# Kernel tuning notes

Measured on AMD Instinct MI355X. Metric: run time of the kernel, lower is better.

The kernel has to match this reference:

```python
import jax, jax.numpy as jnp
import numpy as np

COMMITMENT_COST = 0.25
NUM_EMBEDDINGS = 512
EMBEDDING_DIM = 128


def setup_inputs() -> dict:
    key = jax.random.key(0)
    k1, k2 = jax.random.split(key)
    z = jax.random.normal(k1, (64, 128, 32, 32), dtype=jnp.float32)
    # nn.Embedding weight initialized uniform(-1/K, 1/K)
    lim = 1.0 / NUM_EMBEDDINGS
    emb_weight = jax.random.uniform(
        k2, (NUM_EMBEDDINGS, EMBEDDING_DIM), dtype=jnp.float32,
        minval=-lim, maxval=lim)
    return {"z": z, "emb_weight": emb_weight}


def reference(z, emb_weight):
    b, c, h, w = z.shape  # c == embedding_dim
    # (b, h, w, c) -> (b*h*w, c)
    z_cl = jnp.transpose(z, (0, 2, 3, 1))
    z_flat = z_cl.reshape(b * h * w, c)
    # squared L2 distances: ||z||^2 + ||e||^2 - 2 z.e  -> [N, K]
    distances = (
        jnp.sum(z_flat ** 2, axis=-1, keepdims=True)
        + jnp.sum(emb_weight ** 2, axis=-1)[None, :]
        - 2.0 * jnp.matmul(z_flat, emb_weight.T)
    )
    encoding_indices = jnp.argmin(distances, axis=-1)  # [N]
    z_q = emb_weight[encoding_indices]                 # [N, c]
    z_q = z_q.reshape(b, h, w, c)
    z_q = jnp.transpose(z_q, (0, 3, 1, 2))             # [b, c, h, w]
    loss = (
        jnp.mean((z_q - jax.lax.stop_gradient(z)) ** 2)
        + COMMITMENT_COST * jnp.mean((jax.lax.stop_gradient(z_q) - z) ** 2)
    )
    # straight-through estimator
    z_q_st = z + jax.lax.stop_gradient(z_q - z)
    return (z_q_st, loss, encoding_indices)
```

## Files before the change

### kernel.cpp

```cpp
#include <hip/hip_runtime.h>


#define D_DIM 128
#define HW    1024
#define GAP_THR 4e-4f
#define FLAG_CAP 16384

typedef short short8 __attribute__((ext_vector_type(8)));
typedef float f32x16 __attribute__((ext_vector_type(16)));

union U8 { unsigned int u[4]; short8 s; uint4 q; };

__device__ __forceinline__ unsigned short f2bf(float v) {
    unsigned int u = __builtin_bit_cast(unsigned int, v);
    return (unsigned short)((u + 0x7fffu + ((u >> 16) & 1u)) >> 16);
}
__device__ __forceinline__ unsigned int umn(unsigned int a, unsigned int b) {
    return a < b ? a : b;
}
__device__ __forceinline__ unsigned int umx(unsigned int a, unsigned int b) {
    return a > b ? a : b;
}

__global__ void prep_kernel(const float* __restrict__ emb,
                            float* __restrict__ etr,
                            uint4* __restrict__ ebh,
                            float* __restrict__ se) {
    const int t = blockIdx.x * 256 + threadIdx.x;

    {
        const int k = t >> 7;
        const int d = t & 127;
        etr[d * 512 + k] = emb[t];
    }

    if (t < 8192) {
        const int lane = t & 63;
        const int ks   = (t >> 6) & 7;
        const int kcol = t >> 9;
        const int krow = kcol * 32 + (lane & 31);
        const int d0   = ks * 16 + (lane >> 5) * 8;
        const float* ep = emb + (size_t)krow * D_DIM + d0;
        float v[8];
        #pragma unroll
        for (int j = 0; j < 8; ++j) v[j] = ep[j];
        U8 hh;
        #pragma unroll
        for (int p = 0; p < 4; ++p) {
            const unsigned short h0 = f2bf(v[2*p]), h1 = f2bf(v[2*p+1]);
            hh.u[p] = (unsigned int)h0 | ((unsigned int)h1 << 16);
        }
        ebh[t] = hh.q;
    }

    if (t < 512) {
        const float* e = emb + (size_t)t * D_DIM;
        float r[8];
        #pragma unroll
        for (int j = 0; j < 8; ++j) {
            float v = e[j];
            float p = v * v;
            asm("" : "+v"(p));
            r[j] = p;
        }
        for (int i = 8; i < 128; i += 8) {
            #pragma unroll
            for (int j = 0; j < 8; ++j) {
                float v = e[i + j];
                float p = v * v;
                asm("" : "+v"(p));
                r[j] += p;
            }
        }
        se[t] = ((r[0] + r[1]) + (r[2] + r[3])) + ((r[4] + r[5]) + (r[6] + r[7]));
    }
}

__launch_bounds__(256, 4)
__global__ void dist_kernel(const float* __restrict__ z,
                            const uint4* __restrict__ ebh,
                            const float* __restrict__ se_g,
                            const float* __restrict__ emb,
                            float* __restrict__ idx_out,
                            unsigned int* __restrict__ flag_cnt,
                            int* __restrict__ flag_list,
                            float* __restrict__ zq,
                            double* __restrict__ loss) {
    __shared__ unsigned int red1[2][64], red2[2][64];
    __shared__ int   li_sh[64];
    __shared__ float ept[D_DIM * 33];
    __shared__ float lred[4];

    const int tid  = threadIdx.x;
    const int lane = tid & 63;
    const int wid  = tid >> 6;
    const int wn   = wid >> 1;
    const int wk   = wid & 1;
    const int row  = lane & 31;
    const int bidl = (int)blockIdx.x;
    const int bid  = (bidl & 7) * 128 + (bidl >> 3);
    const int nblk = bid * 64;
    const int bimg = nblk >> 10;
    const int hw0  = nblk & 1023;
    const int hww  = hw0 + wn * 32;

    short8 Ah[8];
    {
        const float* zc = z + (size_t)bimg * (D_DIM * HW) + hww + row;
        #pragma unroll
        for (int ks = 0; ks < 8; ++ks) {
            const int d0 = ks * 16 + (lane >> 5) * 8;
            float v[8];
            #pragma unroll
            for (int j = 0; j < 8; ++j) v[j] = zc[(size_t)(d0 + j) * HW];
            U8 hh;
            #pragma unroll
            for (int p = 0; p < 4; ++p) {
                unsigned int hwd;
                asm("v_cvt_pk_bf16_f32 %0, %1, %2" : "=v"(hwd) : "v"(v[2*p]), "v"(v[2*p+1]));
                hh.u[p] = hwd;
            }
            Ah[ks] = hh.s;
        }
    }

    unsigned int b1[16], b2[16];
    #pragma unroll
    for (int j = 0; j < 16; ++j) { b1[j] = 0xFFFFFFFFu; b2[j] = 0xFFFFFFFFu; }

    #pragma unroll
    for (int i = 0; i < 8; ++i) {
        const int   kc   = wk * 8 + ((i + bidl) & 7);
        const int   kgl  = kc * 32 + row;
        const float sevp = se_g[kgl] + 0.5f;
        const uint4* pbh = ebh + kc * 512 + lane;

        f32x16 acc;
        #pragma unroll
        for (int j = 0; j < 16; ++j) acc[j] = 0.f;

        __builtin_amdgcn_s_setprio(1);
        #pragma unroll
        for (int ks = 0; ks < 8; ++ks) {
            U8 bh; bh.q = pbh[ks * 64];
            acc = __builtin_amdgcn_mfma_f32_32x32x16_bf16(Ah[ks], bh.s, acc, 0, 0, 0);
        }
        __builtin_amdgcn_s_setprio(0);

        #pragma unroll
        for (int j = 0; j < 16; ++j) {
            const float pd = fmaf(-2.f, acc[j], sevp);
            const unsigned int key =
                (__builtin_bit_cast(unsigned int, pd) & 0xFFFFFE00u) | (unsigned int)kgl;
            const unsigned int m = umn(key, b1[j]);
            b2[j] = umn(umx(key, b1[j]), b2[j]);
            b1[j] = m;
        }
    }

    #pragma unroll
    for (int off = 1; off <= 16; off <<= 1) {
        #pragma unroll
        for (int j = 0; j < 16; ++j) {
            const unsigned int o1 = (unsigned int)__shfl_xor((int)b1[j], off);
            const unsigned int o2 = (unsigned int)__shfl_xor((int)b2[j], off);
            const unsigned int m  = umn(b1[j], o1);
            b2[j] = umn(umx(b1[j], o1), umn(b2[j], o2));
            b1[j] = m;
        }
    }

    if ((lane & 31) == 0) {
        const int half = lane >> 5;
        #pragma unroll
        for (int j = 0; j < 16; ++j) {
            const int r = wn * 32 + (j & 3) + 8 * (j >> 2) + 4 * half;
            red1[wk][r] = b1[j];
            red2[wk][r] = b2[j];
        }
    }
    __syncthreads();

    if (tid < 64) {
        const unsigned int v1a = red1[0][tid], v2a = red2[0][tid];
        const unsigned int v1b = red1[1][tid], v2b = red2[1][tid];
        const unsigned int m1 = umn(v1a, v1b);
        const unsigned int m2 = umn(umn(v2a, v2b), umx(v1a, v1b));
        const int n = nblk + tid;
        const int code = (int)(m1 & 511u);
        idx_out[n] = (float)code;
        li_sh[tid] = code;
        const float f1 = __builtin_bit_cast(float, m1 & 0xFFFFFE00u);
        const float f2 = __builtin_bit_cast(float, m2 & 0xFFFFFE00u);
        if (f2 - f1 < GAP_THR) {
            unsigned int p = atomicAdd(flag_cnt, 1u);
            if (p < FLAG_CAP) flag_list[p] = n;
        }
    }

    float lacc = 0.f;
    for (int h = 0; h < 2; ++h) {
        __syncthreads();
        {
            const int p   = tid >> 3;
            const int sub = tid & 7;
            const float* er = emb + (size_t)li_sh[h * 32 + p] * D_DIM + sub * 16;
            #pragma unroll
            for (int j4 = 0; j4 < 4; ++j4) {
                const float4 v = *(const float4*)(er + j4 * 4);
                const int c = sub * 16 + j4 * 4;
                ept[(c + 0) * 33 + p] = v.x;
                ept[(c + 1) * 33 + p] = v.y;
                ept[(c + 2) * 33 + p] = v.z;
                ept[(c + 3) * 33 + p] = v.w;
            }
        }
        __syncthreads();
        {
            const int p  = tid & 31;
            const int c0 = tid >> 5;
            const int hwp = hw0 + h * 32 + p;
            const float* zb2 = z  + (size_t)bimg * (D_DIM * HW) + hwp;
            float*       qb  = zq + (size_t)bimg * (D_DIM * HW) + hwp;
            #pragma unroll
            for (int i = 0; i < 16; ++i) {
                const int c = c0 + i * 8;
                const float v  = ept[c * 33 + p];
                const float zv = zb2[(size_t)c * HW];
                qb[(size_t)c * HW] = v;
                const float df = v - zv;
                lacc = fmaf(df, df, lacc);
            }
        }
    }
    #pragma unroll
    for (int off = 32; off > 0; off >>= 1) lacc += __shfl_down(lacc, off);
    if (lane == 0) lred[wid] = lacc;
    __syncthreads();
    if (tid == 0)
        atomicAdd(loss, (double)(lred[0] + lred[1] + lred[2] + lred[3]));
}

__launch_bounds__(512)
__global__ void fixup_kernel(const float* __restrict__ z,
                             const float* __restrict__ etr,
                             const unsigned int* __restrict__ flag_cnt,
                             const int* __restrict__ flag_list,
                             const float* __restrict__ se_np,
                             float* __restrict__ idx_out) {
    __shared__ float zrow[D_DIM];
    __shared__ float q[D_DIM];
    __shared__ float rsum[8];
    __shared__ float szs;
    __shared__ float rv[8];
    __shared__ int   rix[8];

    const int tid = threadIdx.x;
    unsigned int cnt = *flag_cnt;
    if (cnt > FLAG_CAP) cnt = FLAG_CAP;

    for (unsigned int f = blockIdx.x; f < cnt; f += gridDim.x) {
        const int row = flag_list[f];
        const int b   = row >> 10;
        const int hw  = row & 1023;
        __syncthreads();
        if (tid < D_DIM) {
            float v = z[(size_t)b * (D_DIM * HW) + (size_t)tid * HW + hw];
            zrow[tid] = v;
            q[tid] = v * v;
        }
        __syncthreads();
        if (tid < 8) {
            float r = q[tid];
            for (int i = 8; i < 128; i += 8) r += q[i + tid];
            rsum[tid] = r;
        }
        __syncthreads();
        if (tid == 0)
            szs = ((rsum[0] + rsum[1]) + (rsum[2] + rsum[3]))
                + ((rsum[4] + rsum[5]) + (rsum[6] + rsum[7]));
        __syncthreads();
        const float sz32 = szs;

        const int k = tid;
        double dot0 = 0.0, dot1 = 0.0;
        #pragma unroll 4
        for (int d = 0; d < D_DIM; d += 2) {
            dot0 += (double)etr[d * 512 + k]       * (double)zrow[d];
            dot1 += (double)etr[(d + 1) * 512 + k] * (double)zrow[d + 1];
        }
        const float dotf = (float)(dot0 + dot1);
        const float T    = sz32 + se_np[k];
        float best  = T - 2.0f * dotf;
        int   besti = k;

        #pragma unroll
        for (int off = 32; off > 0; off >>= 1) {
            const float ov = __shfl_down(best, off);
            const int   oi = __shfl_down(besti, off);
            if (ov < best || (ov == best && oi < besti)) { best = ov; besti = oi; }
        }
        if ((tid & 63) == 0) { rv[tid >> 6] = best; rix[tid >> 6] = besti; }
        __syncthreads();
        if (tid == 0) {
            #pragma unroll
            for (int w = 1; w < 8; ++w)
                if (rv[w] < best || (rv[w] == best && rix[w] < besti)) {
                    best = rv[w]; besti = rix[w];
                }
            idx_out[row] = (float)besti;
        }
    }
}

__global__ void fin_kernel(const double* __restrict__ loss, float* __restrict__ out_loss) {
    *out_loss = (float)(*loss * 1.25 / 8388608.0);
}

extern "C" void kernel_launch(void* const* d_in, const int* in_sizes, int n_in,
                              void* d_out, int out_size, void* d_ws, size_t ws_size,
                              hipStream_t stream) {
    const float* z   = (const float*)d_in[0];
    const float* emb = (const float*)d_in[1];
    float* out      = (float*)d_out;
    float* zq       = out;
    float* out_loss = out + 8388608;
    float* idx_f    = out + 8388609;

    char* ws = (char*)d_ws;
    unsigned int* flag_cnt = (unsigned int*)ws;
    double*       loss     = (double*)(ws + 8);
    float*        se       = (float*)(ws + 10240);
    uint4*        ebh      = (uint4*)(ws + 16384);
    int*          flag_list= (int*)(ws + 16384 + 262144);
    float*        etr      = (float*)(ws + 16384 + 262144 + 65536);

    hipMemsetAsync(d_ws, 0, 16384, stream);
    prep_kernel <<<256,  256, 0, stream>>>(emb, etr, ebh, se);
    dist_kernel <<<1024, 256, 0, stream>>>(z, ebh, se, emb, idx_f,
                                           flag_cnt, flag_list, zq, loss);
    fixup_kernel<<<2048, 512, 0, stream>>>(z, etr, flag_cnt, flag_list, se, idx_f);
    fin_kernel  <<<1,    1,   0, stream>>>(loss, out_loss);
}
```

Measured before the change: 98.52 us.

## Split codebook across four waves per 32-row block, doubling grid size

Each block now handles 32 rows instead of 64, and its four waves each scan a quarter of the codebook (4 chunks of 32 codes) rather than two halves for two row groups. The cross-wave top-2 merge becomes a four-way reduction, the gather/write epilogue runs in a single pass, and the grid doubles to 2048 blocks. The aim is more blocks and shorter per-wave dependency chains, for better occupancy and latency hiding. In exchange, codebook B-fragments are re-read by twice as many blocks, and more atomics hit the loss accumulator.

Measured after the change: 118.8 us. 1.21x slower.

```diff
diff --git a/kernel.cpp b/kernel.cpp
--- a/kernel.cpp
+++ b/kernel.cpp
@@ -86,27 +86,24 @@
                             int* __restrict__ flag_list,
                             float* __restrict__ zq,
                             double* __restrict__ loss) {
-    __shared__ unsigned int red1[2][64], red2[2][64];
-    __shared__ int   li_sh[64];
+    __shared__ unsigned int red1[4][32], red2[4][32];
+    __shared__ int   li_sh[32];
     __shared__ float ept[D_DIM * 33];
     __shared__ float lred[4];
 
     const int tid  = threadIdx.x;
     const int lane = tid & 63;
     const int wid  = tid >> 6;
-    const int wn   = wid >> 1;
-    const int wk   = wid & 1;
     const int row  = lane & 31;
     const int bidl = (int)blockIdx.x;
-    const int bid  = (bidl & 7) * 128 + (bidl >> 3);
-    const int nblk = bid * 64;
+    const int bid  = (bidl & 7) * 256 + (bidl >> 3);
+    const int nblk = bid * 32;
     const int bimg = nblk >> 10;
     const int hw0  = nblk & 1023;
-    const int hww  = hw0 + wn * 32;
 
     short8 Ah[8];
     {
-        const float* zc = z + (size_t)bimg * (D_DIM * HW) + hww + row;
+        const float* zc = z + (size_t)bimg * (D_DIM * HW) + hw0 + row;
         #pragma unroll
         for (int ks = 0; ks < 8; ++ks) {
             const int d0 = ks * 16 + (lane >> 5) * 8;
@@ -128,9 +125,8 @@
     #pragma unroll
     for (int j = 0; j < 16; ++j) { b1[j] = 0xFFFFFFFFu; b2[j] = 0xFFFFFFFFu; }
 
-    #pragma unroll
-    for (int i = 0; i < 8; ++i) {
-        const int   kc   = wk * 8 + ((i + bidl) & 7);
+    for (int i = 0; i < 4; ++i) {
+        const int   kc   = wid * 4 + ((i + bidl) & 3);
         const int   kgl  = kc * 32 + row;
         const float sevp = se_g[kgl] + 0.5f;
         const uint4* pbh = ebh + kc * 512 + lane;
@@ -174,18 +170,23 @@
         const int half = lane >> 5;
         #pragma unroll
         for (int j = 0; j < 16; ++j) {
-            const int r = wn * 32 + (j & 3) + 8 * (j >> 2) + 4 * half;
-            red1[wk][r] = b1[j];
-            red2[wk][r] = b2[j];
+            const int r = (j & 3) + 8 * (j >> 2) + 4 * half;
+            red1[wid][r] = b1[j];
+            red2[wid][r] = b2[j];
         }
     }
     __syncthreads();
 
-    if (tid < 64) {
-        const unsigned int v1a = red1[0][tid], v2a = red2[0][tid];
-        const unsigned int v1b = red1[1][tid], v2b = red2[1][tid];
-        const unsigned int m1 = umn(v1a, v1b);
-        const unsigned int m2 = umn(umn(v2a, v2b), umx(v1a, v1b));
+    if (tid < 32) {
+        unsigned int m1 = red1[0][tid], m2 = red2[0][tid];
+        #pragma unroll
+        for (int w = 1; w < 4; ++w) {
+            const unsigned int v1 = red1[w][tid];
+            const unsigned int v2 = red2[w][tid];
+            const unsigned int nm = umn(m1, v1);
+            m2 = umn(umn(m2, v2), umx(m1, v1));
+            m1 = nm;
+        }
         const int n = nblk + tid;
         const int code = (int)(m1 & 511u);
         idx_out[n] = (float)code;
@@ -197,45 +198,42 @@
             if (p < FLAG_CAP) flag_list[p] = n;
         }
     }
-
-    float lacc = 0.f;
-    for (int h = 0; h < 2; ++h) {
-        __syncthreads();
-        {
-            const int p   = tid >> 3;
-            const int sub = tid & 7;
-            const float* er = emb + (size_t)li_sh[h * 32 + p] * D_DIM + sub * 16;
-            #pragma unroll
-            for (int j4 = 0; j4 < 4; ++j4) {
-                const float4 v = *(const float4*)(er + j4 * 4);
-                const int c = sub * 16 + j4 * 4;
-                ept[(c + 0) * 33 + p] = v.x;
-                ept[(c + 1) * 33 + p] = v.y;
-                ept[(c + 2) * 33 + p] = v.z;
-                ept[(c + 3) * 33 + p] = v.w;
-            }
-        }
-        __syncthreads();
-        {
-            const int p  = tid & 31;
-            const int c0 = tid >> 5;
-            const int hwp = hw0 + h * 32 + p;
-            const float* zb2 = z  + (size_t)bimg * (D_DIM * HW) + hwp;
-            float*       qb  = zq + (size_t)bimg * (D_DIM * HW) + hwp;
-            #pragma unroll
-            for (int i = 0; i < 16; ++i) {
-                const int c = c0 + i * 8;
-                const float v  = ept[c * 33 + p];
-                const float zv = zb2[(size_t)c * HW];
-                qb[(size_t)c * HW] = v;
-                const float df = v - zv;
-                lacc = fmaf(df, df, lacc);
-            }
-        }
-    }
-    #pragma unroll
-    for (int off = 32; off > 0; off >>= 1) lacc += __shfl_down(lacc, off);
-    if (lane == 0) lred[wid] = lacc;
+    __syncthreads();
+
+    {
+        const int p   = tid >> 3;
+        const int sub = tid & 7;
+        const float* er = emb + (size_t)li_sh[p] * D_DIM + sub * 16;
+        #pragma unroll
+        for (int j4 = 0; j4 < 4; ++j4) {
+            const float4 v = *(const float4*)(er + j4 * 4);
+            const int c = sub * 16 + j4 * 4;
+            ept[(c + 0) * 33 + p] = v.x;
+            ept[(c + 1) * 33 + p] = v.y;
+            ept[(c + 2) * 33 + p] = v.z;
+            ept[(c + 3) * 33 + p] = v.w;
+        }
+    }
+    __syncthreads();
+    {
+        const int p  = tid & 31;
+        const int c0 = tid >> 5;
+        const float* zb2 = z  + (size_t)bimg * (D_DIM * HW) + hw0 + p;
+        float*       qb  = zq + (size_t)bimg * (D_DIM * HW) + hw0 + p;
+        float lacc = 0.f;
+        #pragma unroll
+        for (int i = 0; i < 16; ++i) {
+            const int c = c0 + i * 8;
+            const float v  = ept[c * 33 + p];
+            const float zv = zb2[(size_t)c * HW];
+            qb[(size_t)c * HW] = v;
+            const float df = v - zv;
+            lacc = fmaf(df, df, lacc);
+        }
+        #pragma unroll
+        for (int off = 32; off > 0; off >>= 1) lacc += __shfl_down(lacc, off);
+        if (lane == 0) lred[wid] = lacc;
+    }
     __syncthreads();
     if (tid == 0)
         atomicAdd(loss, (double)(lred[0] + lred[1] + lred[2] + lred[3]));
@@ -337,7 +335,7 @@
 
     hipMemsetAsync(d_ws, 0, 16384, stream);
     prep_kernel <<<256,  256, 0, stream>>>(emb, etr, ebh, se);
-    dist_kernel <<<1024, 256, 0, stream>>>(z, ebh, se, emb, idx_f,
+    dist_kernel <<<2048, 256, 0, stream>>>(z, ebh, se, emb, idx_f,
                                            flag_cnt, flag_list, zq, loss);
     fixup_kernel<<<2048, 512, 0, stream>>>(z, etr, flag_cnt, flag_list, se, idx_f);
     fin_kernel  <<<1,    1,   0, stream>>>(loss, out_loss);
```
